# Optimization experiments

Hardware: AMD Instinct MI355X
Metric: run time of the kernel (lower is better)

The kernel has to match this reference:

```python
import jax, jax.numpy as jnp
import numpy as np

H = 16
D_MODEL = 1024
HEAD_DIM = D_MODEL // H
NEG = -1e9


def setup_inputs() -> dict:
    key = jax.random.key(0)
    k1, k2, k3, k4, k5, k6 = jax.random.split(key, 6)
    B, L = 2, 2048
    feature = jax.random.normal(k1, (B, L, D_MODEL), dtype=jnp.float32)
    mask = jax.random.randint(k2, (B, L), 0, 2, dtype=jnp.int32)
    # Linear weights stored torch-style as [out, in]; biases zero-init per initialize().
    s = 1.0 / np.sqrt(D_MODEL)
    W_Q = jax.random.uniform(k3, (D_MODEL, D_MODEL), jnp.float32, -s, s)
    W_K = jax.random.uniform(k4, (D_MODEL, D_MODEL), jnp.float32, -s, s)
    W_V = jax.random.uniform(k5, (D_MODEL, D_MODEL), jnp.float32, -s, s)
    b_Q = jnp.zeros((D_MODEL,), jnp.float32)
    b_K = jnp.zeros((D_MODEL,), jnp.float32)
    b_V = jnp.zeros((D_MODEL,), jnp.float32)
    return {"feature": feature, "mask": mask, "W_Q": W_Q, "b_Q": b_Q,
            "W_K": W_K, "b_K": b_K, "W_V": W_V, "b_V": b_V}


def reference(feature, mask, W_Q, b_Q, W_K, b_K, W_V, b_V):
    B, L, _ = feature.shape
    scale = jnp.sqrt(jnp.float32(HEAD_DIM))
    # Projections: torch Linear is x @ W^T + b. Split into heads: [B, H, L, Dh]
    def proj(W, b):
        y = feature @ W.T + b
        return y.reshape(B, L, H, HEAD_DIM).transpose(0, 2, 1, 3)
    Q = proj(W_Q, b_Q)
    K = proj(W_K, b_K)
    V = proj(W_V, b_V)
    # Scores [B, H, Lq, Lk]
    A = jnp.einsum('bhqd,bhkd->bhqk', Q, K) / scale
    # Key-side mask broadcast over heads and query positions
    A = jnp.where(mask[:, None, None, :] == 0, jnp.float32(NEG), A)
    alpha = jax.nn.softmax(A, axis=-1)
    out = jnp.einsum('bhqk,bhkd->bhqd', alpha, V)  # [B, H, L, Dh]
    return out.transpose(0, 2, 1, 3).reshape(B, L, H * HEAD_DIM)
```

## Files before the change

kernel.cpp:

```cpp
#include <hip/hip_runtime.h>

typedef __bf16 bf16;
typedef __attribute__((ext_vector_type(8))) __bf16 bf16x8;
typedef __attribute__((ext_vector_type(4))) float f32x4;
typedef unsigned int u32;

#define D_MODEL 1024
#define SEQ_L   2048
#define NHEAD   16
#define HDIM    64
#define MROWS   4096

#define FEAT_OFF  512u
#define VT_OFF    FEAT_OFF
#define WQ_OFF    (FEAT_OFF + 4194304u)
#define WK_OFF    (WQ_OFF + 1048576u)
#define WV_OFF    (WK_OFF + 1048576u)
#define BQ_OFF    (WV_OFF + 1048576u)
#define BK_OFF    (BQ_OFF + 1024u)
#define BV_OFF    (BK_OFF + 1024u)
#define Q_OFF     (BV_OFF + 1024u)
#define K_OFF     (Q_OFF + 4194304u)
#define V_OFF     (K_OFF + 4194304u)

__device__ __forceinline__ bf16 f2bf(float f) {
    unsigned u = __builtin_bit_cast(unsigned, f);
    unsigned r = (u + 0x7fffu + ((u >> 16) & 1u)) >> 16;
    unsigned short s = (unsigned short)r;
    return __builtin_bit_cast(bf16, s);
}

typedef const __attribute__((address_space(1))) u32* gp_t;
typedef __attribute__((address_space(3))) u32* lp_t;
__device__ __forceinline__ void ld16(const bf16* g, bf16* l) {
    __builtin_amdgcn_global_load_lds((gp_t)g, (lp_t)l, 16, 0, 0);
}

__global__ void convert_in(const float* __restrict__ feat,
                           const float* __restrict__ wq, const float* __restrict__ wk,
                           const float* __restrict__ wv,
                           const float* __restrict__ bq, const float* __restrict__ bk,
                           const float* __restrict__ bv,
                           bf16* __restrict__ ws) {
    const float* src; bf16* dst; int n;
    switch (blockIdx.y) {
        case 0: src = feat; dst = ws + FEAT_OFF; n = 4194304; break;
        case 1: src = wq;   dst = ws + WQ_OFF;   n = 1048576; break;
        case 2: src = wk;   dst = ws + WK_OFF;   n = 1048576; break;
        case 3: src = wv;   dst = ws + WV_OFF;   n = 1048576; break;
        case 4: src = bq;   dst = ws + BQ_OFF;   n = 1024;    break;
        case 5: src = bk;   dst = ws + BK_OFF;   n = 1024;    break;
        default: src = bv;  dst = ws + BV_OFF;   n = 1024;    break;
    }
    int idx = (blockIdx.x * 256 + threadIdx.x) * 4;
    if (idx >= n) return;
    float4 v = ((const float4*)src)[idx >> 2];
    dst[idx + 0] = f2bf(v.x);
    dst[idx + 1] = f2bf(v.y);
    dst[idx + 2] = f2bf(v.z);
    dst[idx + 3] = f2bf(v.w);
}

__global__ __launch_bounds__(256, 2) void qkv_gemm(const bf16* __restrict__ ws,
                                                   bf16* __restrict__ wsw) {
    const int zi = blockIdx.z;
    const bf16* X    = ws + FEAT_OFF;
    const bf16* W    = ws + ((zi == 0) ? WQ_OFF : (zi == 1) ? WK_OFF : WV_OFF);
    const bf16* bias = ws + ((zi == 0) ? BQ_OFF : (zi == 1) ? BK_OFF : BV_OFF);
    bf16* Y = wsw + Q_OFF + (size_t)zi * MROWS * D_MODEL;

    __shared__ bf16 Alds[128 * 64];
    __shared__ bf16 Blds[128 * 64];

    const int t    = threadIdx.x;
    const int lane = t & 63;
    const int wave = t >> 6;
    const int quad = lane >> 4;
    const int l16  = lane & 15;
    const int m0   = blockIdx.x * 128;
    const int n0   = blockIdx.y * 128;
    const int wrow = (wave >> 1) * 64;
    const int wcol = (wave & 1) * 64;

    const int r8 = lane >> 3;
    const int sl = lane & 7;
    const int sg = sl ^ r8;

    f32x4 acc[4][4];
    for (int mi = 0; mi < 4; ++mi)
        for (int ni = 0; ni < 4; ++ni)
            acc[mi][ni] = (f32x4){0.f, 0.f, 0.f, 0.f};

    for (int k0 = 0; k0 < D_MODEL; k0 += 64) {
#pragma unroll
        for (int i = 0; i < 4; ++i) {
            int ch  = wave * 4 + i;
            int row = ch * 8 + r8;
            ld16(X + (size_t)(m0 + row) * D_MODEL + k0 + sg * 8, Alds + ch * 512);
            ld16(W + (size_t)(n0 + row) * D_MODEL + k0 + sg * 8, Blds + ch * 512);
        }
        __syncthreads();

#pragma unroll
        for (int kk = 0; kk < 2; ++kk) {
            const int sgb = quad + kk * 4;
            bf16x8 af[4], bfr[4];
#pragma unroll
            for (int mi = 0; mi < 4; ++mi) {
                int row = wrow + mi * 16 + l16;
                af[mi] = *(const bf16x8*)(&Alds[row * 64 + ((sgb ^ (row & 7)) << 3)]);
            }
#pragma unroll
            for (int ni = 0; ni < 4; ++ni) {
                int row = wcol + ni * 16 + l16;
                bfr[ni] = *(const bf16x8*)(&Blds[row * 64 + ((sgb ^ (row & 7)) << 3)]);
            }
#pragma unroll
            for (int mi = 0; mi < 4; ++mi)
#pragma unroll
                for (int ni = 0; ni < 4; ++ni)
                    acc[mi][ni] = __builtin_amdgcn_mfma_f32_16x16x32_bf16(
                        af[mi], bfr[ni], acc[mi][ni], 0, 0, 0);
        }
        __syncthreads();
    }

#pragma unroll
    for (int ni = 0; ni < 4; ++ni) {
        int col = n0 + wcol + ni * 16 + l16;
        float bvf = (float)bias[col];
#pragma unroll
        for (int mi = 0; mi < 4; ++mi) {
            int rowb = m0 + wrow + mi * 16 + quad * 4;
#pragma unroll
            for (int r = 0; r < 4; ++r)
                Y[(size_t)(rowb + r) * D_MODEL + col] = f2bf(acc[mi][ni][r] + bvf);
        }
    }
}

__global__ void transpose_v(const bf16* __restrict__ ws, bf16* __restrict__ wsw) {
    const bf16* V = ws + V_OFF;
    bf16* Vt = wsw + VT_OFF;
    const int tt = blockIdx.x, bh = blockIdx.y;
    const int b = bh >> 4, h = bh & 15;
    const int t = threadIdx.x;
    __shared__ bf16 T[64 * 72];

#pragma unroll
    for (int i = 0; i < 2; ++i) {
        int c = t + 256 * i;
        int row = c >> 3, seg = c & 7;
        uint4 v = *(const uint4*)(V + (size_t)(b * SEQ_L + tt * 64 + row) * D_MODEL + h * 64 + seg * 8);
        *(uint4*)(&T[row * 72 + seg * 8]) = v;
    }
    __syncthreads();
#pragma unroll
    for (int i = 0; i < 2; ++i) {
        int c = t + 256 * i;
        int d = c >> 3, sg = c & 7;
        unsigned short pk[8];
#pragma unroll
        for (int j = 0; j < 8; ++j)
            pk[j] = ((const unsigned short*)T)[(sg * 8 + j) * 72 + d];
        *(uint4*)(Vt + ((size_t)bh * 64 + d) * SEQ_L + tt * 64 + sg * 8) = *(const uint4*)pk;
    }
}

#define ALDP 72
#define PLDP 68

__global__ __launch_bounds__(256, 2) void attn_kernel(
    const bf16* __restrict__ ws, const int* __restrict__ mask,
    float* __restrict__ out) {
    const int qt = blockIdx.x;
    const int bh = blockIdx.y;
    const int b  = bh >> 4, h = bh & 15;
    const int t    = threadIdx.x;
    const int lane = t & 63;
    const int wave = t >> 6;
    const int quad = lane >> 4;
    const int l16  = lane & 15;

    __shared__ bf16 Klds[64 * ALDP];
    __shared__ bf16 Vlds[64 * ALDP];
    __shared__ float mlds[64];
    __shared__ bf16 Plds[4][16 * PLDP];

    const size_t headoff = ((size_t)b * SEQ_L) * D_MODEL + h * HDIM;
    const bf16* Qh  = ws + Q_OFF + headoff;
    const bf16* Kh  = ws + K_OFF + headoff;
    const bf16* Vth = ws + VT_OFF + (size_t)bh * 64 * SEQ_L;

    const int qrow = qt * 64 + wave * 16 + l16;
    bf16x8 qf[2];
    qf[0] = *(const bf16x8*)(Qh + (size_t)qrow * D_MODEL + quad * 8);
    qf[1] = *(const bf16x8*)(Qh + (size_t)qrow * D_MODEL + 32 + quad * 8);
#pragma unroll
    for (int j = 0; j < 8; ++j) {
        qf[0][j] = (bf16)((float)qf[0][j] * 0.125f);
        qf[1][j] = (bf16)((float)qf[1][j] * 0.125f);
    }

    bf16x8 vone;
#pragma unroll
    for (int j = 0; j < 8; ++j) vone[j] = (bf16)1.0f;

    f32x4 o[4];
    for (int ti = 0; ti < 4; ++ti) o[ti] = (f32x4){0.f, 0.f, 0.f, 0.f};
    f32x4 lacc = (f32x4){0.f, 0.f, 0.f, 0.f};

    for (int kt = 0; kt < SEQ_L; kt += 64) {
#pragma unroll
        for (int i = 0; i < 2; ++i) {
            int c = t + 256 * i;
            int row = c >> 3, seg = c & 7;
            uint4 kv = *(const uint4*)(Kh + (size_t)(kt + row) * D_MODEL + seg * 8);
            *(uint4*)(&Klds[row * ALDP + seg * 8]) = kv;
            uint4 vv = *(const uint4*)(Vth + (size_t)row * SEQ_L + kt + seg * 8);
            *(uint4*)(&Vlds[row * ALDP + seg * 8]) = vv;
        }
        if (t < 64) mlds[t] = (mask[b * SEQ_L + kt + t] != 0) ? 0.f : -1e9f;
        __syncthreads();

        f32x4 s[4];
#pragma unroll
        for (int ni = 0; ni < 4; ++ni) {
            s[ni] = (f32x4){0.f, 0.f, 0.f, 0.f};
            bf16x8 kf0 = *(const bf16x8*)(&Klds[(ni * 16 + l16) * ALDP + quad * 8]);
            bf16x8 kf1 = *(const bf16x8*)(&Klds[(ni * 16 + l16) * ALDP + 32 + quad * 8]);
            s[ni] = __builtin_amdgcn_mfma_f32_16x16x32_bf16(qf[0], kf0, s[ni], 0, 0, 0);
            s[ni] = __builtin_amdgcn_mfma_f32_16x16x32_bf16(qf[1], kf1, s[ni], 0, 0, 0);
        }

#pragma unroll
        for (int ni = 0; ni < 4; ++ni) {
            float mb = mlds[ni * 16 + l16];
#pragma unroll
            for (int r = 0; r < 4; ++r) {
                float p = __expf(s[ni][r] + mb);
                Plds[wave][(quad * 4 + r) * PLDP + ni * 16 + l16] = f2bf(p);
            }
        }

        bf16x8 pf0 = *(const bf16x8*)(&Plds[wave][l16 * PLDP + quad * 8]);
        bf16x8 pf1 = *(const bf16x8*)(&Plds[wave][l16 * PLDP + 32 + quad * 8]);
        lacc = __builtin_amdgcn_mfma_f32_16x16x32_bf16(pf0, vone, lacc, 0, 0, 0);
        lacc = __builtin_amdgcn_mfma_f32_16x16x32_bf16(pf1, vone, lacc, 0, 0, 0);
#pragma unroll
        for (int ti = 0; ti < 4; ++ti) {
            bf16x8 vf0 = *(const bf16x8*)(&Vlds[(ti * 16 + l16) * ALDP + quad * 8]);
            bf16x8 vf1 = *(const bf16x8*)(&Vlds[(ti * 16 + l16) * ALDP + 32 + quad * 8]);
            o[ti] = __builtin_amdgcn_mfma_f32_16x16x32_bf16(pf0, vf0, o[ti], 0, 0, 0);
            o[ti] = __builtin_amdgcn_mfma_f32_16x16x32_bf16(pf1, vf1, o[ti], 0, 0, 0);
        }
        __syncthreads();
    }

    float rl[4];
#pragma unroll
    for (int r = 0; r < 4; ++r) rl[r] = 1.0f / fmaxf(lacc[r], 1e-30f);
#pragma unroll
    for (int ti = 0; ti < 4; ++ti) {
#pragma unroll
        for (int r = 0; r < 4; ++r) {
            int q = qt * 64 + wave * 16 + quad * 4 + r;
            int d = h * HDIM + ti * 16 + l16;
            out[((size_t)(b * SEQ_L + q)) * D_MODEL + d] = o[ti][r] * rl[r];
        }
    }
}

extern "C" void kernel_launch(void* const* d_in, const int* in_sizes, int n_in,
                              void* d_out, int out_size, void* d_ws, size_t ws_size,
                              hipStream_t stream) {
    const float* feat = (const float*)d_in[0];
    const int*   mask = (const int*)d_in[1];
    const float* Wq = (const float*)d_in[2];
    const float* bq = (const float*)d_in[3];
    const float* Wk = (const float*)d_in[4];
    const float* bk = (const float*)d_in[5];
    const float* Wv = (const float*)d_in[6];
    const float* bv = (const float*)d_in[7];

    bf16* ws = (bf16*)d_ws;

    dim3 gc(4096, 7);
    convert_in<<<gc, 256, 0, stream>>>(feat, Wq, Wk, Wv, bq, bk, bv, ws);

    dim3 g1(MROWS / 128, D_MODEL / 128, 3);
    qkv_gemm<<<g1, 256, 0, stream>>>(ws, ws);

    dim3 gt(SEQ_L / 64, 2 * NHEAD);
    transpose_v<<<gt, 256, 0, stream>>>(ws, ws);

    dim3 g2(SEQ_L / 64, 2 * NHEAD);
    attn_kernel<<<g2, 256, 0, stream>>>(ws, mask, (float*)d_out);
}
```

Before: 193.1 us.

## Produce transposed V directly from GEMM and use 32x32 MFMA attention

The V projection is computed as W_V·X^T so the GEMM writes V already transposed per head, which removes the separate transpose kernel and its extra global-memory pass. The attention kernel now runs two waves of 32 query rows each and uses 32x32x16 MFMA tiles. The row sum is accumulated in registers and reduced with cross-lane shuffles instead of an extra MFMA against a ones vector. In exchange, blocks drop to 128 threads, which may lower occupancy, and the V GEMM epilogue writes with a strided pattern.

```diff
diff --git a/kernel.cpp b/kernel.cpp
--- a/kernel.cpp
+++ b/kernel.cpp
@@ -3,6 +3,7 @@
 typedef __bf16 bf16;
 typedef __attribute__((ext_vector_type(8))) __bf16 bf16x8;
 typedef __attribute__((ext_vector_type(4))) float f32x4;
+typedef __attribute__((ext_vector_type(16))) float f32x16;
 typedef unsigned int u32;
 
 #define D_MODEL 1024
@@ -12,7 +13,6 @@
 #define MROWS   4096
 
 #define FEAT_OFF  512u
-#define VT_OFF    FEAT_OFF
 #define WQ_OFF    (FEAT_OFF + 4194304u)
 #define WK_OFF    (WQ_OFF + 1048576u)
 #define WV_OFF    (WK_OFF + 1048576u)
@@ -64,10 +64,10 @@
 __global__ __launch_bounds__(256, 2) void qkv_gemm(const bf16* __restrict__ ws,
                                                    bf16* __restrict__ wsw) {
     const int zi = blockIdx.z;
-    const bf16* X    = ws + FEAT_OFF;
-    const bf16* W    = ws + ((zi == 0) ? WQ_OFF : (zi == 1) ? WK_OFF : WV_OFF);
+    const bf16* Amat = (zi == 2) ? ws + WV_OFF : ws + FEAT_OFF;
+    const bf16* Bmat = (zi == 0) ? ws + WQ_OFF : (zi == 1) ? ws + WK_OFF : ws + FEAT_OFF;
     const bf16* bias = ws + ((zi == 0) ? BQ_OFF : (zi == 1) ? BK_OFF : BV_OFF);
-    bf16* Y = wsw + Q_OFF + (size_t)zi * MROWS * D_MODEL;
+    bf16* Y = (zi == 2) ? wsw + V_OFF : wsw + Q_OFF + (size_t)zi * 4194304u;
 
     __shared__ bf16 Alds[128 * 64];
     __shared__ bf16 Blds[128 * 64];
@@ -77,8 +77,8 @@
     const int wave = t >> 6;
     const int quad = lane >> 4;
     const int l16  = lane & 15;
-    const int m0   = blockIdx.x * 128;
-    const int n0   = blockIdx.y * 128;
+    const int m0   = ((zi == 2) ? blockIdx.y : blockIdx.x) * 128;
+    const int n0   = ((zi == 2) ? blockIdx.x : blockIdx.y) * 128;
     const int wrow = (wave >> 1) * 64;
     const int wcol = (wave & 1) * 64;
 
@@ -96,8 +96,8 @@
         for (int i = 0; i < 4; ++i) {
             int ch  = wave * 4 + i;
             int row = ch * 8 + r8;
-            ld16(X + (size_t)(m0 + row) * D_MODEL + k0 + sg * 8, Alds + ch * 512);
-            ld16(W + (size_t)(n0 + row) * D_MODEL + k0 + sg * 8, Blds + ch * 512);
+            ld16(Amat + (size_t)(m0 + row) * D_MODEL + k0 + sg * 8, Alds + ch * 512);
+            ld16(Bmat + (size_t)(n0 + row) * D_MODEL + k0 + sg * 8, Blds + ch * 512);
         }
         __syncthreads();
 
@@ -125,52 +125,42 @@
         __syncthreads();
     }
 
-#pragma unroll
-    for (int ni = 0; ni < 4; ++ni) {
-        int col = n0 + wcol + ni * 16 + l16;
-        float bvf = (float)bias[col];
+    if (zi < 2) {
+#pragma unroll
+        for (int ni = 0; ni < 4; ++ni) {
+            int col = n0 + wcol + ni * 16 + l16;
+            float bvf = (float)bias[col];
+#pragma unroll
+            for (int mi = 0; mi < 4; ++mi) {
+                int rowb = m0 + wrow + mi * 16 + quad * 4;
+#pragma unroll
+                for (int r = 0; r < 4; ++r)
+                    Y[(size_t)(rowb + r) * D_MODEL + col] = f2bf(acc[mi][ni][r] + bvf);
+            }
+        }
+    } else {
 #pragma unroll
         for (int mi = 0; mi < 4; ++mi) {
-            int rowb = m0 + wrow + mi * 16 + quad * 4;
-#pragma unroll
-            for (int r = 0; r < 4; ++r)
-                Y[(size_t)(rowb + r) * D_MODEL + col] = f2bf(acc[mi][ni][r] + bvf);
-        }
-    }
-}
-
-__global__ void transpose_v(const bf16* __restrict__ ws, bf16* __restrict__ wsw) {
-    const bf16* V = ws + V_OFF;
-    bf16* Vt = wsw + VT_OFF;
-    const int tt = blockIdx.x, bh = blockIdx.y;
-    const int b = bh >> 4, h = bh & 15;
-    const int t = threadIdx.x;
-    __shared__ bf16 T[64 * 72];
-
-#pragma unroll
-    for (int i = 0; i < 2; ++i) {
-        int c = t + 256 * i;
-        int row = c >> 3, seg = c & 7;
-        uint4 v = *(const uint4*)(V + (size_t)(b * SEQ_L + tt * 64 + row) * D_MODEL + h * 64 + seg * 8);
-        *(uint4*)(&T[row * 72 + seg * 8]) = v;
-    }
-    __syncthreads();
-#pragma unroll
-    for (int i = 0; i < 2; ++i) {
-        int c = t + 256 * i;
-        int d = c >> 3, sg = c & 7;
-        unsigned short pk[8];
-#pragma unroll
-        for (int j = 0; j < 8; ++j)
-            pk[j] = ((const unsigned short*)T)[(sg * 8 + j) * 72 + d];
-        *(uint4*)(Vt + ((size_t)bh * 64 + d) * SEQ_L + tt * 64 + sg * 8) = *(const uint4*)pk;
-    }
-}
-
-#define ALDP 72
-#define PLDP 68
-
-__global__ __launch_bounds__(256, 2) void attn_kernel(
+#pragma unroll
+            for (int r = 0; r < 4; ++r) {
+                int rowv = m0 + wrow + mi * 16 + quad * 4 + r;
+                float bvf = (float)bias[rowv];
+#pragma unroll
+                for (int ni = 0; ni < 4; ++ni) {
+                    int col = n0 + wcol + ni * 16 + l16;
+                    size_t addr = (size_t)(col >> 11) * 2097152u +
+                                  (size_t)rowv * 2048u + (col & 2047);
+                    Y[addr] = f2bf(acc[mi][ni][r] + bvf);
+                }
+            }
+        }
+    }
+}
+
+#define KSTR 68
+#define PSTR 68
+
+__global__ __launch_bounds__(128, 2) void attn_kernel(
     const bf16* __restrict__ ws, const int* __restrict__ mask,
     float* __restrict__ out) {
     const int qt = blockIdx.x;
@@ -179,95 +169,95 @@
     const int t    = threadIdx.x;
     const int lane = t & 63;
     const int wave = t >> 6;
-    const int quad = lane >> 4;
-    const int l16  = lane & 15;
-
-    __shared__ bf16 Klds[64 * ALDP];
-    __shared__ bf16 Vlds[64 * ALDP];
+    const int half = lane >> 5;
+    const int l32  = lane & 31;
+
+    __shared__ bf16 Klds[64 * KSTR];
+    __shared__ bf16 Vlds[64 * KSTR];
+    __shared__ bf16 Plds[2][32 * PSTR];
     __shared__ float mlds[64];
-    __shared__ bf16 Plds[4][16 * PLDP];
-
-    const size_t headoff = ((size_t)b * SEQ_L) * D_MODEL + h * HDIM;
-    const bf16* Qh  = ws + Q_OFF + headoff;
-    const bf16* Kh  = ws + K_OFF + headoff;
-    const bf16* Vth = ws + VT_OFF + (size_t)bh * 64 * SEQ_L;
-
-    const int qrow = qt * 64 + wave * 16 + l16;
-    bf16x8 qf[2];
-    qf[0] = *(const bf16x8*)(Qh + (size_t)qrow * D_MODEL + quad * 8);
-    qf[1] = *(const bf16x8*)(Qh + (size_t)qrow * D_MODEL + 32 + quad * 8);
-#pragma unroll
-    for (int j = 0; j < 8; ++j) {
-        qf[0][j] = (bf16)((float)qf[0][j] * 0.125f);
-        qf[1][j] = (bf16)((float)qf[1][j] * 0.125f);
-    }
-
-    bf16x8 vone;
-#pragma unroll
-    for (int j = 0; j < 8; ++j) vone[j] = (bf16)1.0f;
-
-    f32x4 o[4];
-    for (int ti = 0; ti < 4; ++ti) o[ti] = (f32x4){0.f, 0.f, 0.f, 0.f};
-    f32x4 lacc = (f32x4){0.f, 0.f, 0.f, 0.f};
+
+    const bf16* Qh  = ws + Q_OFF + (size_t)(b * SEQ_L) * D_MODEL + h * HDIM;
+    const bf16* Kh  = ws + K_OFF + (size_t)(b * SEQ_L) * D_MODEL + h * HDIM;
+    const bf16* Vth = ws + V_OFF + (size_t)b * 2097152u + (size_t)(h * HDIM) * SEQ_L;
+
+    const int qrow = qt * 64 + wave * 32 + l32;
+    bf16x8 qf[4];
+#pragma unroll
+    for (int ks = 0; ks < 4; ++ks) {
+        qf[ks] = *(const bf16x8*)(Qh + (size_t)qrow * D_MODEL + ks * 16 + half * 8);
+#pragma unroll
+        for (int j = 0; j < 8; ++j)
+            qf[ks][j] = (bf16)((float)qf[ks][j] * 0.125f);
+    }
+
+    f32x16 o0, o1;
+    float lsum[16];
+#pragma unroll
+    for (int i = 0; i < 16; ++i) { o0[i] = 0.f; o1[i] = 0.f; lsum[i] = 0.f; }
 
     for (int kt = 0; kt < SEQ_L; kt += 64) {
 #pragma unroll
-        for (int i = 0; i < 2; ++i) {
-            int c = t + 256 * i;
+        for (int i = 0; i < 4; ++i) {
+            int c = t + 128 * i;
             int row = c >> 3, seg = c & 7;
             uint4 kv = *(const uint4*)(Kh + (size_t)(kt + row) * D_MODEL + seg * 8);
-            *(uint4*)(&Klds[row * ALDP + seg * 8]) = kv;
+            *(uint4*)(&Klds[row * KSTR + seg * 8]) = kv;
             uint4 vv = *(const uint4*)(Vth + (size_t)row * SEQ_L + kt + seg * 8);
-            *(uint4*)(&Vlds[row * ALDP + seg * 8]) = vv;
+            *(uint4*)(&Vlds[row * KSTR + seg * 8]) = vv;
         }
         if (t < 64) mlds[t] = (mask[b * SEQ_L + kt + t] != 0) ? 0.f : -1e9f;
         __syncthreads();
 
-        f32x4 s[4];
-#pragma unroll
-        for (int ni = 0; ni < 4; ++ni) {
-            s[ni] = (f32x4){0.f, 0.f, 0.f, 0.f};
-            bf16x8 kf0 = *(const bf16x8*)(&Klds[(ni * 16 + l16) * ALDP + quad * 8]);
-            bf16x8 kf1 = *(const bf16x8*)(&Klds[(ni * 16 + l16) * ALDP + 32 + quad * 8]);
-            s[ni] = __builtin_amdgcn_mfma_f32_16x16x32_bf16(qf[0], kf0, s[ni], 0, 0, 0);
-            s[ni] = __builtin_amdgcn_mfma_f32_16x16x32_bf16(qf[1], kf1, s[ni], 0, 0, 0);
-        }
-
-#pragma unroll
-        for (int ni = 0; ni < 4; ++ni) {
-            float mb = mlds[ni * 16 + l16];
-#pragma unroll
-            for (int r = 0; r < 4; ++r) {
-                float p = __expf(s[ni][r] + mb);
-                Plds[wave][(quad * 4 + r) * PLDP + ni * 16 + l16] = f2bf(p);
-            }
-        }
-
-        bf16x8 pf0 = *(const bf16x8*)(&Plds[wave][l16 * PLDP + quad * 8]);
-        bf16x8 pf1 = *(const bf16x8*)(&Plds[wave][l16 * PLDP + 32 + quad * 8]);
-        lacc = __builtin_amdgcn_mfma_f32_16x16x32_bf16(pf0, vone, lacc, 0, 0, 0);
-        lacc = __builtin_amdgcn_mfma_f32_16x16x32_bf16(pf1, vone, lacc, 0, 0, 0);
-#pragma unroll
-        for (int ti = 0; ti < 4; ++ti) {
-            bf16x8 vf0 = *(const bf16x8*)(&Vlds[(ti * 16 + l16) * ALDP + quad * 8]);
-            bf16x8 vf1 = *(const bf16x8*)(&Vlds[(ti * 16 + l16) * ALDP + 32 + quad * 8]);
-            o[ti] = __builtin_amdgcn_mfma_f32_16x16x32_bf16(pf0, vf0, o[ti], 0, 0, 0);
-            o[ti] = __builtin_amdgcn_mfma_f32_16x16x32_bf16(pf1, vf1, o[ti], 0, 0, 0);
-        }
-        __syncthreads();
-    }
-
-    float rl[4];
-#pragma unroll
-    for (int r = 0; r < 4; ++r) rl[r] = 1.0f / fmaxf(lacc[r], 1e-30f);
-#pragma unroll
-    for (int ti = 0; ti < 4; ++ti) {
-#pragma unroll
-        for (int r = 0; r < 4; ++r) {
-            int q = qt * 64 + wave * 16 + quad * 4 + r;
-            int d = h * HDIM + ti * 16 + l16;
-            out[((size_t)(b * SEQ_L + q)) * D_MODEL + d] = o[ti][r] * rl[r];
-        }
+        f32x16 s0, s1;
+#pragma unroll
+        for (int i = 0; i < 16; ++i) { s0[i] = 0.f; s1[i] = 0.f; }
+#pragma unroll
+        for (int ks = 0; ks < 4; ++ks) {
+            bf16x8 kf0 = *(const bf16x8*)(&Klds[l32 * KSTR + ks * 16 + half * 8]);
+            bf16x8 kf1 = *(const bf16x8*)(&Klds[(32 + l32) * KSTR + ks * 16 + half * 8]);
+            s0 = __builtin_amdgcn_mfma_f32_32x32x16_bf16(qf[ks], kf0, s0, 0, 0, 0);
+            s1 = __builtin_amdgcn_mfma_f32_32x32x16_bf16(qf[ks], kf1, s1, 0, 0, 0);
+        }
+
+        const float mb0 = mlds[l32];
+        const float mb1 = mlds[32 + l32];
+#pragma unroll
+        for (int reg = 0; reg < 16; ++reg) {
+            int row = (reg & 3) + 8 * (reg >> 2) + 4 * half;
+            float p0 = __expf(s0[reg] + mb0);
+            float p1 = __expf(s1[reg] + mb1);
+            lsum[reg] += p0 + p1;
+            Plds[wave][row * PSTR + l32]      = (bf16)p0;
+            Plds[wave][row * PSTR + 32 + l32] = (bf16)p1;
+        }
+
+#pragma unroll
+        for (int ks = 0; ks < 4; ++ks) {
+            bf16x8 pf  = *(const bf16x8*)(&Plds[wave][l32 * PSTR + ks * 16 + half * 8]);
+            bf16x8 vf0 = *(const bf16x8*)(&Vlds[l32 * KSTR + ks * 16 + half * 8]);
+            bf16x8 vf1 = *(const bf16x8*)(&Vlds[(32 + l32) * KSTR + ks * 16 + half * 8]);
+            o0 = __builtin_amdgcn_mfma_f32_32x32x16_bf16(pf, vf0, o0, 0, 0, 0);
+            o1 = __builtin_amdgcn_mfma_f32_32x32x16_bf16(pf, vf1, o1, 0, 0, 0);
+        }
+        __syncthreads();
+    }
+
+#pragma unroll
+    for (int reg = 0; reg < 16; ++reg) {
+#pragma unroll
+        for (int off = 1; off < 32; off <<= 1)
+            lsum[reg] += __shfl_xor(lsum[reg], off);
+        lsum[reg] = 1.0f / fmaxf(lsum[reg], 1e-30f);
+    }
+
+#pragma unroll
+    for (int reg = 0; reg < 16; ++reg) {
+        int row = (reg & 3) + 8 * (reg >> 2) + 4 * half;
+        int q = qt * 64 + wave * 32 + row;
+        size_t base = ((size_t)(b * SEQ_L + q)) * D_MODEL + h * HDIM;
+        out[base + l32]      = o0[reg] * lsum[reg];
+        out[base + 32 + l32] = o1[reg] * lsum[reg];
     }
 }
 
@@ -288,12 +278,9 @@
     dim3 gc(4096, 7);
     convert_in<<<gc, 256, 0, stream>>>(feat, Wq, Wk, Wv, bq, bk, bv, ws);
 
-    dim3 g1(MROWS / 128, D_MODEL / 128, 3);
+    dim3 g1(32, 8, 3);
     qkv_gemm<<<g1, 256, 0, stream>>>(ws, ws);
 
-    dim3 gt(SEQ_L / 64, 2 * NHEAD);
-    transpose_v<<<gt, 256, 0, stream>>>(ws, ws);
-
     dim3 g2(SEQ_L / 64, 2 * NHEAD);
-    attn_kernel<<<g2, 256, 0, stream>>>(ws, mask, (float*)d_out);
-}
+    attn_kernel<<<g2, 128, 0, stream>>>(ws, mask, (float*)d_out);
+}
```

Result: no change. 192.8 us (-0.2%).
